# Optimization experiments

Hardware: AMD Instinct MI355X
Metric: run time of the kernel (lower is better)

Reference implementation:

```python
import jax, jax.numpy as jnp
import numpy as np

# Model dims (match init_kwargs / input_specs)
L = 2      # layer_dim
B = 64     # batch
T = 512    # max seq len
D = 256    # input_dim (== hidden_dim, required by stacked wiring)
H = 256    # hidden_dim
O = 2      # output_dim


def setup_inputs() -> dict:
    key = jax.random.key(0)
    ks = jax.random.split(key, 10)
    s = 1.0 / np.sqrt(H)
    f32 = jnp.float32
    return {
        "x_data": jax.random.normal(ks[0], (B, T, D), f32),
        "x_length": jax.random.randint(ks[1], (B,), 1, T + 1),
        "x_label": jax.random.uniform(ks[2], (B,), f32),
        # Per-layer GRU-cell weights, stacked over layers (bias=False).
        "Wz": (jax.random.normal(ks[3], (L, D, H), f32) * s),
        "Uz": (jax.random.normal(ks[4], (L, H, H), f32) * s),
        "Wr": (jax.random.normal(ks[5], (L, D, H), f32) * s),
        "Ur": (jax.random.normal(ks[6], (L, H, H), f32) * s),
        "Wh": (jax.random.normal(ks[7], (L, D, H), f32) * s),
        "Uh": (jax.random.normal(ks[8], (L, H, H), f32) * s),
        # Output projection of the last layer (only last layer's `out` is used).
        "Wo": (jax.random.normal(ks[9], (H, O), f32) * s),
    }


def reference(x_data, x_length, x_label, Wz, Uz, Wr, Ur, Wh, Uh, Wo):
    # Training-mode forward: sum over batch and valid timesteps of
    # (label - sigmoid(out[:, 1]))**2, with per-layer states S1, S2
    # carried across time. Vectorized over batch; lax.scan over time.
    Tn = x_data.shape[1]
    xs = jnp.swapaxes(x_data, 0, 1)  # [T, B, D]
    S1_0 = jnp.zeros((L, B, H), x_data.dtype)
    S2_0 = jnp.zeros((L, B, H), x_data.dtype)

    def step(carry, xt):
        S1, S2 = carry
        inp = xt  # [B, D]
        for l in range(L):  # small fixed layer loop
            z = jax.nn.sigmoid(inp @ Wz[l] + S1[l] @ Uz[l])
            r = jax.nn.sigmoid(inp @ Wr[l] + S1[l] @ Ur[l])
            h = jnp.tanh(inp @ Wh[l] + (r * S1[l]) @ Uh[l])
            hn = (1.0 - z) * S1[l] + z * h          # new hidden (S1)
            S2n = z * S2[l] + (1.0 - z) * h          # secondary memory (S2)
            S1 = S1.at[l].set(hn)
            S2 = S2.at[l].set(S2n)
            inp = hn
        score = jax.nn.sigmoid((inp @ Wo)[:, 1])     # out[:, 1] -> [B]
        return (S1, S2), score

    _, scores = jax.lax.scan(step, (S1_0, S2_0), xs)  # [T, B]
    mask = (jnp.arange(Tn)[:, None] < x_length[None, :]).astype(scores.dtype)
    loss = jnp.sum(mask * (x_label[None, :] - scores) ** 2)
    return loss
```

## Files before the change

kernel.cpp:

```cpp
#include <hip/hip_runtime.h>

#define LAY 2
#define BATCH 64
#define TMAX 512
#define DIM 256
#define AST 264
#define CHUNK 16

typedef float floatx4 __attribute__((ext_vector_type(4)));
typedef __bf16 bf16x8 __attribute__((ext_vector_type(8)));
#define MFMA_FP8  __builtin_amdgcn_mfma_f32_16x16x32_fp8_fp8
#define MFMA_BF16 __builtin_amdgcn_mfma_f32_16x16x32_bf16

#define BAR_LDS() asm volatile("s_waitcnt lgkmcnt(0)\n\ts_barrier" ::: "memory")

#define OFF_WPW 0xA0000
#define OFF_FLG 0x150000
#define OFF_XP  0x200000
#define OFF_HP  0x1C00000
#define OFF_HN  0x3600000

__device__ __forceinline__ unsigned short f2bf(float f) {
    unsigned int u = __float_as_uint(f);
    unsigned int r = u + 0x7fffu + ((u >> 16) & 1u);
    return (unsigned short)(r >> 16);
}
__device__ __forceinline__ unsigned int pk2(float a, float b) {
    return (unsigned int)__builtin_amdgcn_cvt_pk_fp8_f32(a, b, 0, false);
}
__device__ __forceinline__ unsigned char f2q(float a) { return (unsigned char)(pk2(a, a) & 0xff); }
__device__ __forceinline__ void unp4(unsigned int u, float* f) {
    auto lo = __builtin_amdgcn_cvt_pk_f32_fp8((int)u, false);
    auto hi = __builtin_amdgcn_cvt_pk_f32_fp8((int)u, true);
    f[0] = lo[0]; f[1] = lo[1]; f[2] = hi[0]; f[3] = hi[1];
}
__device__ __forceinline__ float sigf(float x) {
    return __builtin_amdgcn_rcpf(1.f + __expf(-x));
}
__device__ __forceinline__ float tanhfast2y(float twoy) { return 2.f * sigf(twoy) - 1.f; }

__device__ __forceinline__ void ast_u32(unsigned int* p, unsigned int v) {
    __hip_atomic_store(p, v, __ATOMIC_RELAXED, __HIP_MEMORY_SCOPE_AGENT);
}

__global__ void prep_weights(const float* __restrict__ Wz, const float* __restrict__ Wr,
                             const float* __restrict__ Wh, const float* __restrict__ Uz,
                             const float* __restrict__ Ur, const float* __restrict__ Uh,
                             unsigned char* __restrict__ ws, float* __restrict__ out) {
    int T = blockIdx.x * 256 + threadIdx.x;
    if (T == 0) out[0] = 0.f;
    if (T < 192) ((int*)(ws + OFF_FLG))[T] = 0;
    if (T < 294912) {
        int e = T & 3, half = (T >> 2) & 1, lane = (T >> 3) & 63;
        int kp = (T >> 9) & 3, nt = (T >> 11) & 15, mu = T >> 15;
        const float* s;
        if (mu < 6) {
            int g = mu % 3, l = mu / 3;
            s = (g == 0 ? Uz : g == 1 ? Ur : Uh) + l * 65536;
        } else {
            int g = mu - 6;
            s = (g == 0 ? Wz : g == 1 ? Wr : Wh) + 65536;
        }
        int n  = nt * 16 + (lane & 15);
        int k0 = (2 * kp + half) * 32 + (lane >> 4) * 8 + 2 * e;
        float w0 = s[(k0 << 8) + n] * 8.f;
        float w1 = s[((k0 + 1) << 8) + n] * 8.f;
        int addr = ((mu * 16 + nt) * 4 + kp) * 1024 + lane * 16 + half * 8 + 2 * e;
        *(unsigned short*)(ws + addr) = (unsigned short)(pk2(w0, w1) & 0xffff);
    } else {
        int T2 = T - 294912;
        int e = T2 & 3, lane = (T2 >> 2) & 63;
        int kf = (T2 >> 8) & 7, nt = (T2 >> 11) & 15, mw = T2 >> 15;
        const float* s = (mw == 0 ? Wz : mw == 1 ? Wr : Wh);
        int n  = nt * 16 + (lane & 15);
        int k0 = kf * 32 + (lane >> 4) * 8 + 2 * e;
        unsigned int v = (unsigned int)f2bf(s[(k0 << 8) + n]) |
                         ((unsigned int)f2bf(s[((k0 + 1) << 8) + n]) << 16);
        int addr = ((mw * 16 + nt) * 8 + kf) * 1024 + lane * 16 + 4 * e;
        *(unsigned int*)(ws + OFF_WPW + addr) = v;
    }
}

template <int SCORE, int WMODE, int POST>
__device__ __forceinline__ void scan_body(
    const unsigned int* __restrict__ xp, const unsigned char* __restrict__ wpU,
    int lbase, int bg, unsigned char* __restrict__ hnout,
    const int* __restrict__ xlen, const float* __restrict__ xlab,
    const float* __restrict__ Wo, float* __restrict__ out,
    int* wflags, int* pflag,
    unsigned char (*s1q)[AST], unsigned char (*rsq)[AST], float (*s1o)[264],
    float* wo1s, int* s_rdy, int tmax)
{
    const int tid = threadIdx.x, wave = tid >> 6, lane = tid & 63;
    const int l15 = lane & 15, quad = lane >> 4;
    const int b0 = bg * 16;

    for (int i = tid; i < 16 * AST; i += 1024) ((unsigned char*)s1q)[i] = 0;
    if (SCORE && tid < DIM) wo1s[tid] = Wo[2 * tid + 1];
    const int lenr = xlen[b0 + l15];
    const float labr = SCORE ? xlab[b0 + l15] : 0.f;
    (void)lenr; (void)labr;

    const int nt = wave;
    const int colA = nt * 16 + l15, rowb = quad * 4;

    long uz[8], ur[8], uh[8];
    {
        const unsigned char* pz = wpU + (size_t)(((lbase + 0) * 16 + nt) * 4) * 1024 + lane * 16;
        const unsigned char* pr = wpU + (size_t)(((lbase + 1) * 16 + nt) * 4) * 1024 + lane * 16;
        const unsigned char* ph = wpU + (size_t)(((lbase + 2) * 16 + nt) * 4) * 1024 + lane * 16;
#pragma unroll
        for (int kf = 0; kf < 8; ++kf) {
            int o = (kf >> 1) * 1024 + (kf & 1) * 8;
            uz[kf] = *(const long*)(pz + o);
            ur[kf] = *(const long*)(pr + o);
            uh[kf] = *(const long*)(ph + o);
        }
    }
    float s1r[4] = {};
    float accl = 0.f;
    int ready = 0;
    __syncthreads();

    for (int t = 0; t < tmax; ++t) {
        if constexpr (WMODE == 1) {
            if (t >= ready) {
                if (tid == 0) {
                    int vv, g = 0;
                    for (;;) {
                        vv = 1 << 30;
#pragma unroll
                        for (int q = 0; q < 4; ++q) {
                            int m = __hip_atomic_load(wflags + q, __ATOMIC_RELAXED, __HIP_MEMORY_SCOPE_AGENT);
                            vv = m < vv ? m : vv;
                        }
                        if (vv > t || ++g > (1 << 19)) break;
                        __builtin_amdgcn_s_sleep(2);
                    }
                    __threadfence();
                    *s_rdy = vv > t ? vv : t + 1;
                }
                __syncthreads();
                ready = *s_rdy;
            }
        } else if constexpr (WMODE == 2) {
            if (t >= ready) {
                if (tid == 0) {
                    const int ch = t >> 4;
                    int g = 0;
                    for (;;) {
                        int c = __hip_atomic_load(wflags + ch, __ATOMIC_RELAXED, __HIP_MEMORY_SCOPE_AGENT);
                        if (c >= 16 || ++g > (1 << 19)) break;
                        __builtin_amdgcn_s_sleep(2);
                    }
                    __threadfence();
                    *s_rdy = (ch + 1) * CHUNK;
                }
                __syncthreads();
                ready = *s_rdy;
            }
        }

        const unsigned int* xpt = xp + (size_t)(bg * 512 + t) * 3072 + lane;
        unsigned int xz = xpt[nt * 64];
        unsigned int xr = xpt[1024 + nt * 64];
        unsigned int xh = xpt[2048 + nt * 64];

        long sf[8];
#pragma unroll
        for (int kf = 0; kf < 8; ++kf) sf[kf] = *(const long*)&s1q[l15][kf * 32 + quad * 8];
        floatx4 za = {0.f, 0.f, 0.f, 0.f}, ra = za;
#pragma unroll
        for (int kf = 0; kf < 8; ++kf) {
            ra = MFMA_FP8(sf[kf], ur[kf], ra, 0, 0, 0);
            za = MFMA_FP8(sf[kf], uz[kf], za, 0, 0, 0);
        }
        float xrf[4];
        unp4(xr, xrf);
#pragma unroll
        for (int i = 0; i < 4; ++i) {
            float r = sigf(0.125f * ra[i] + 0.0625f * xrf[i]);
            rsq[rowb + i][colA] = f2q(r * s1r[i]);
        }
        BAR_LDS();

        long rf[8];
#pragma unroll
        for (int kf = 0; kf < 8; ++kf) rf[kf] = *(const long*)&rsq[l15][kf * 32 + quad * 8];
        floatx4 ha = {0.f, 0.f, 0.f, 0.f};
#pragma unroll
        for (int kf = 0; kf < 8; ++kf) ha = MFMA_FP8(rf[kf], uh[kf], ha, 0, 0, 0);
        float xzf[4], xhf[4];
        unp4(xz, xzf); unp4(xh, xhf);
#pragma unroll
        for (int i = 0; i < 4; ++i) {
            float z = sigf(0.125f * za[i] + 0.0625f * xzf[i]);
            float h = tanhfast2y(0.25f * ha[i] + 0.125f * xhf[i]);
            float hn = (1.f - z) * s1r[i] + z * h;
            s1r[i] = hn;
            s1q[rowb + i][colA] = f2q(hn);
            if (SCORE) s1o[rowb + i][colA] = hn;
        }
        BAR_LDS();

        if (!SCORE) {
            const int r = tid >> 6, c = (tid & 63) * 4;
            unsigned int v4 = *(const unsigned int*)&s1q[r][c];
            *(unsigned int*)(hnout + ((size_t)(b0 + r) * 512 + t) * 256 + c) = v4;
        } else if (wave == 0) {
            const int row = l15, c0 = quad * 64;
            float p = 0.f;
#pragma unroll
            for (int u = 0; u < 64; u += 4) {
                float4 sv = *(const float4*)&s1o[row][c0 + u];
                float4 wv = *(const float4*)&wo1s[c0 + u];
                p = fmaf(sv.x, wv.x, p); p = fmaf(sv.y, wv.y, p);
                p = fmaf(sv.z, wv.z, p); p = fmaf(sv.w, wv.w, p);
            }
            p += __shfl_xor(p, 16);
            p += __shfl_xor(p, 32);
            if (lane < 16 && t < lenr) {
                float sc = sigf(p);
                float d = labr - sc;
                accl = fmaf(d, d, accl);
            }
        }

        if (POST && (((t & (CHUNK - 1)) == (CHUNK - 1)) || t == tmax - 1)) {
            __syncthreads();
            if (tid == 0) {
                __threadfence();
                __hip_atomic_store(pflag, t + 1, __ATOMIC_RELEASE, __HIP_MEMORY_SCOPE_AGENT);
            }
        }
    }

    if (SCORE && wave == 0) {
        accl += __shfl_xor(accl, 1);
        accl += __shfl_xor(accl, 2);
        accl += __shfl_xor(accl, 4);
        accl += __shfl_xor(accl, 8);
        if (lane == 0) atomicAdd(out, accl);
    }
}

__global__ __launch_bounds__(1024, 4) void fused_pipeline(
    const float* __restrict__ x,
    unsigned int* __restrict__ XP, unsigned int* __restrict__ HP,
    const unsigned char* __restrict__ wpU, const unsigned char* __restrict__ wpW,
    unsigned char* __restrict__ HN,
    const int* __restrict__ xlen, const float* __restrict__ xlab,
    const float* __restrict__ Wo, float* __restrict__ out, int* flags)
{
    __shared__ __align__(16) unsigned char s1q[16][AST];
    __shared__ __align__(16) unsigned char rsq[16][AST];
    __shared__ __align__(16) float s1o[16][264];
    __shared__ float wo1s[DIM];
    __shared__ int s_rdy;

    const int bid = blockIdx.x;
    const int tid = threadIdx.x, wave = tid >> 6, lane = tid & 63;
    const int l15 = lane & 15, quad = lane >> 4;
    int* cnt = flags + 32;

    if (bid >= 24) {
        const int idx = bid - 24;
        const int pt = idx & 511, pbg = idx >> 9;
        const float* s = x + ((size_t)(pbg * 16 + l15) * 512 + pt) * 256;
        bf16x8 af[8];
#pragma unroll
        for (int kf = 0; kf < 8; ++kf) {
            float4 a = *(const float4*)(s + kf * 32 + quad * 8);
            float4 b = *(const float4*)(s + kf * 32 + quad * 8 + 4);
            union { unsigned short u[8]; bf16x8 v; } cv;
            cv.u[0] = f2bf(a.x); cv.u[1] = f2bf(a.y); cv.u[2] = f2bf(a.z); cv.u[3] = f2bf(a.w);
            cv.u[4] = f2bf(b.x); cv.u[5] = f2bf(b.y); cv.u[6] = f2bf(b.z); cv.u[7] = f2bf(b.w);
            af[kf] = cv.v;
        }
        floatx4 az = {0.f, 0.f, 0.f, 0.f}, ar = az, ah = az;
        const unsigned char* bz = wpW + (size_t)((0 * 16 + wave) * 8) * 1024 + lane * 16;
        const unsigned char* br = wpW + (size_t)((1 * 16 + wave) * 8) * 1024 + lane * 16;
        const unsigned char* bh = wpW + (size_t)((2 * 16 + wave) * 8) * 1024 + lane * 16;
#pragma unroll
        for (int kf = 0; kf < 8; ++kf) {
            az = MFMA_BF16(af[kf], *(const bf16x8*)(bz + kf * 1024), az, 0, 0, 0);
            ar = MFMA_BF16(af[kf], *(const bf16x8*)(br + kf * 1024), ar, 0, 0, 0);
            ah = MFMA_BF16(af[kf], *(const bf16x8*)(bh + kf * 1024), ah, 0, 0, 0);
        }
        const size_t ob = (size_t)(pbg * 512 + pt) * 3072 + wave * 64 + lane;
        ast_u32(&XP[ob],        pk2(16.f * az[0], 16.f * az[1]) | (pk2(16.f * az[2], 16.f * az[3]) << 16));
        ast_u32(&XP[ob + 1024], pk2(16.f * ar[0], 16.f * ar[1]) | (pk2(16.f * ar[2], 16.f * ar[3]) << 16));
        ast_u32(&XP[ob + 2048], pk2(16.f * ah[0], 16.f * ah[1]) | (pk2(16.f * ah[2], 16.f * ah[3]) << 16));
        __syncthreads();
        if (tid == 0)
            __hip_atomic_fetch_add(cnt + pbg * 32 + (pt >> 4), 1,
                                   __ATOMIC_RELAXED, __HIP_MEMORY_SCOPE_AGENT);
        return;
    }

    int role, bg, p = 0;
    if (bid < 4)       { role = 0; bg = bid; }
    else if (bid < 20) { role = 1; bg = (bid - 4) >> 2; p = (bid - 4) & 3; }
    else               { role = 2; bg = bid - 20; }
    const int b0 = bg * 16;

    int v = xlen[b0 + l15];
#pragma unroll
    for (int o = 1; o < 16; o <<= 1) v = max(v, __shfl_xor(v, o));
    const int tmax = __builtin_amdgcn_readfirstlane(v);

    if (role == 0) {
        scan_body<0, 2, 1>(XP, wpU, 0, bg, HN, xlen, xlab, Wo, out,
                           cnt + bg * 32, flags + bg, s1q, rsq, s1o, wo1s, &s_rdy, tmax);
    } else if (role == 2) {
        scan_body<1, 1, 0>(HP, wpU, 3, bg, nullptr, xlen, xlab, Wo, out,
                           flags + 4 + bg * 4, nullptr, s1q, rsq, s1o, wo1s, &s_rdy, tmax);
    } else {
        int* wf = flags + bg;
        int* pf = flags + 4 + bg * 4 + p;
        const unsigned char* bz = wpU + (size_t)((6 * 16 + wave) * 4) * 1024 + lane * 16;
        const unsigned char* br = wpU + (size_t)((7 * 16 + wave) * 4) * 1024 + lane * 16;
        const unsigned char* bh = wpU + (size_t)((8 * 16 + wave) * 4) * 1024 + lane * 16;
        for (int base = 0; base < tmax; base += CHUNK) {
            const int target = (base + CHUNK < tmax) ? base + CHUNK : tmax;
            if (tid == 0) {
                int vv, g = 0;
                for (;;) {
                    vv = __hip_atomic_load(wf, __ATOMIC_RELAXED, __HIP_MEMORY_SCOPE_AGENT);
                    if (vv >= target || ++g > (1 << 19)) break;
                    __builtin_amdgcn_s_sleep(2);
                }
                __threadfence();
            }
            __syncthreads();

            const int t0 = base + p * 4;
            const int t1 = (t0 + 4 < tmax) ? t0 + 4 : tmax;
            for (int t = t0; t < t1; ++t) {
                const unsigned char* sA = HN + ((size_t)(b0 + l15) * 512 + t) * 256;
                long af[8];
#pragma unroll
                for (int kf = 0; kf < 8; ++kf) af[kf] = *(const long*)(sA + kf * 32 + quad * 8);
                floatx4 az = {0.f, 0.f, 0.f, 0.f}, ar = az, ah = az;
#pragma unroll
                for (int kf = 0; kf < 8; ++kf) {
                    int o = (kf >> 1) * 1024 + (kf & 1) * 8;
                    az = MFMA_FP8(af[kf], *(const long*)(bz + o), az, 0, 0, 0);
                    ar = MFMA_FP8(af[kf], *(const long*)(br + o), ar, 0, 0, 0);
                    ah = MFMA_FP8(af[kf], *(const long*)(bh + o), ah, 0, 0, 0);
                }
                const size_t ob = (size_t)(bg * 512 + t) * 3072 + wave * 64 + lane;
                HP[ob]        = pk2(2.f * az[0], 2.f * az[1]) | (pk2(2.f * az[2], 2.f * az[3]) << 16);
                HP[ob + 1024] = pk2(2.f * ar[0], 2.f * ar[1]) | (pk2(2.f * ar[2], 2.f * ar[3]) << 16);
                HP[ob + 2048] = pk2(2.f * ah[0], 2.f * ah[1]) | (pk2(2.f * ah[2], 2.f * ah[3]) << 16);
            }

            __syncthreads();
            if (tid == 0) {
                __threadfence();
                __hip_atomic_store(pf, base + CHUNK, __ATOMIC_RELEASE, __HIP_MEMORY_SCOPE_AGENT);
            }
        }
    }
}

extern "C" void kernel_launch(void* const* d_in, const int* in_sizes, int n_in,
                              void* d_out, int out_size, void* d_ws, size_t ws_size,
                              hipStream_t stream) {
    const float* x    = (const float*)d_in[0];
    const int*   xlen = (const int*)d_in[1];
    const float* xlab = (const float*)d_in[2];
    const float* Wz   = (const float*)d_in[3];
    const float* Uz   = (const float*)d_in[4];
    const float* Wr   = (const float*)d_in[5];
    const float* Ur   = (const float*)d_in[6];
    const float* Wh   = (const float*)d_in[7];
    const float* Uh   = (const float*)d_in[8];
    const float* Wo   = (const float*)d_in[9];
    float* out = (float*)d_out;

    unsigned char* ws  = (unsigned char*)d_ws;
    unsigned char* wpU = ws;
    unsigned char* wpW = ws + OFF_WPW;
    int*           FLG = (int*)(ws + OFF_FLG);
    unsigned int*  XP  = (unsigned int*)(ws + OFF_XP);
    unsigned int*  HP  = (unsigned int*)(ws + OFF_HP);
    unsigned char* HN  = ws + OFF_HN;

    prep_weights<<<1536, 256, 0, stream>>>(Wz, Wr, Wh, Uz, Ur, Uh, ws, out);
    fused_pipeline<<<2072, 1024, 0, stream>>>(x, XP, HP, wpU, wpW, HN,
                                              xlen, xlab, Wo, out, FLG);
}
```

Measured before the change: 1.233 ms.

## Quantize recurrent weights in-kernel and interleave projected-input layout

The prep kernel no longer packs the FP8 U matrices or the layer-1 W matrices. Each scan and projection block now loads fp32 weights straight into registers and quantizes them once at startup, which shrinks the prep launch and drops a workspace round trip. The per-timestep XP/HP buffers are interleaved so the z, r and h values for a lane sit next to each other, and the hidden update uses an fma form. The trade-off is strided uncoalesced fp32 weight loads in every block's prologue, repeated across the many blocks.

Measured after the change: 1.126 ms. 8.7% less time.

```diff
diff --git a/kernel.cpp b/kernel.cpp
--- a/kernel.cpp
+++ b/kernel.cpp
@@ -43,48 +43,41 @@
     __hip_atomic_store(p, v, __ATOMIC_RELAXED, __HIP_MEMORY_SCOPE_AGENT);
 }
 
+__device__ __forceinline__ long quant8(const float* s) {
+    unsigned int p01 = pk2(8.f * s[0 * 256], 8.f * s[1 * 256]);
+    unsigned int p23 = pk2(8.f * s[2 * 256], 8.f * s[3 * 256]);
+    unsigned int p45 = pk2(8.f * s[4 * 256], 8.f * s[5 * 256]);
+    unsigned int p67 = pk2(8.f * s[6 * 256], 8.f * s[7 * 256]);
+    unsigned long long v = (unsigned long long)(p01 & 0xffffu)
+                         | ((unsigned long long)(p23 & 0xffffu) << 16)
+                         | ((unsigned long long)(p45 & 0xffffu) << 32)
+                         | ((unsigned long long)(p67 & 0xffffu) << 48);
+    return (long)v;
+}
+
 __global__ void prep_weights(const float* __restrict__ Wz, const float* __restrict__ Wr,
-                             const float* __restrict__ Wh, const float* __restrict__ Uz,
-                             const float* __restrict__ Ur, const float* __restrict__ Uh,
+                             const float* __restrict__ Wh,
                              unsigned char* __restrict__ ws, float* __restrict__ out) {
     int T = blockIdx.x * 256 + threadIdx.x;
     if (T == 0) out[0] = 0.f;
     if (T < 192) ((int*)(ws + OFF_FLG))[T] = 0;
-    if (T < 294912) {
-        int e = T & 3, half = (T >> 2) & 1, lane = (T >> 3) & 63;
-        int kp = (T >> 9) & 3, nt = (T >> 11) & 15, mu = T >> 15;
-        const float* s;
-        if (mu < 6) {
-            int g = mu % 3, l = mu / 3;
-            s = (g == 0 ? Uz : g == 1 ? Ur : Uh) + l * 65536;
-        } else {
-            int g = mu - 6;
-            s = (g == 0 ? Wz : g == 1 ? Wr : Wh) + 65536;
-        }
-        int n  = nt * 16 + (lane & 15);
-        int k0 = (2 * kp + half) * 32 + (lane >> 4) * 8 + 2 * e;
-        float w0 = s[(k0 << 8) + n] * 8.f;
-        float w1 = s[((k0 + 1) << 8) + n] * 8.f;
-        int addr = ((mu * 16 + nt) * 4 + kp) * 1024 + lane * 16 + half * 8 + 2 * e;
-        *(unsigned short*)(ws + addr) = (unsigned short)(pk2(w0, w1) & 0xffff);
-    } else {
-        int T2 = T - 294912;
-        int e = T2 & 3, lane = (T2 >> 2) & 63;
-        int kf = (T2 >> 8) & 7, nt = (T2 >> 11) & 15, mw = T2 >> 15;
-        const float* s = (mw == 0 ? Wz : mw == 1 ? Wr : Wh);
-        int n  = nt * 16 + (lane & 15);
-        int k0 = kf * 32 + (lane >> 4) * 8 + 2 * e;
-        unsigned int v = (unsigned int)f2bf(s[(k0 << 8) + n]) |
-                         ((unsigned int)f2bf(s[((k0 + 1) << 8) + n]) << 16);
-        int addr = ((mw * 16 + nt) * 8 + kf) * 1024 + lane * 16 + 4 * e;
-        *(unsigned int*)(ws + OFF_WPW + addr) = v;
-    }
+    int e = T & 3, lane = (T >> 2) & 63;
+    int kf = (T >> 8) & 7, nt = (T >> 11) & 15, mw = T >> 15;
+    const float* s = (mw == 0 ? Wz : mw == 1 ? Wr : Wh);
+    int n  = nt * 16 + (lane & 15);
+    int k0 = kf * 32 + (lane >> 4) * 8 + 2 * e;
+    unsigned int v = (unsigned int)f2bf(s[(k0 << 8) + n]) |
+                     ((unsigned int)f2bf(s[((k0 + 1) << 8) + n]) << 16);
+    int addr = ((mw * 16 + nt) * 8 + kf) * 1024 + lane * 16 + 4 * e;
+    *(unsigned int*)(ws + OFF_WPW + addr) = v;
 }
 
 template <int SCORE, int WMODE, int POST>
 __device__ __forceinline__ void scan_body(
-    const unsigned int* __restrict__ xp, const unsigned char* __restrict__ wpU,
-    int lbase, int bg, unsigned char* __restrict__ hnout,
+    const unsigned int* __restrict__ xp,
+    const float* __restrict__ Uzs, const float* __restrict__ Urs,
+    const float* __restrict__ Uhs,
+    int bg, unsigned char* __restrict__ hnout,
     const int* __restrict__ xlen, const float* __restrict__ xlab,
     const float* __restrict__ Wo, float* __restrict__ out,
     int* wflags, int* pflag,
@@ -106,15 +99,13 @@
 
     long uz[8], ur[8], uh[8];
     {
-        const unsigned char* pz = wpU + (size_t)(((lbase + 0) * 16 + nt) * 4) * 1024 + lane * 16;
-        const unsigned char* pr = wpU + (size_t)(((lbase + 1) * 16 + nt) * 4) * 1024 + lane * 16;
-        const unsigned char* ph = wpU + (size_t)(((lbase + 2) * 16 + nt) * 4) * 1024 + lane * 16;
+        const int nb = nt * 16 + l15;
 #pragma unroll
         for (int kf = 0; kf < 8; ++kf) {
-            int o = (kf >> 1) * 1024 + (kf & 1) * 8;
-            uz[kf] = *(const long*)(pz + o);
-            ur[kf] = *(const long*)(pr + o);
-            uh[kf] = *(const long*)(ph + o);
+            const size_t kb = (size_t)(kf * 32 + quad * 8) * 256 + nb;
+            uz[kf] = quant8(Uzs + kb);
+            ur[kf] = quant8(Urs + kb);
+            uh[kf] = quant8(Uhs + kb);
         }
     }
     float s1r[4] = {};
@@ -161,10 +152,10 @@
             }
         }
 
-        const unsigned int* xpt = xp + (size_t)(bg * 512 + t) * 3072 + lane;
-        unsigned int xz = xpt[nt * 64];
-        unsigned int xr = xpt[1024 + nt * 64];
-        unsigned int xh = xpt[2048 + nt * 64];
+        const unsigned int* xpt = xp + ((size_t)(bg * 512 + t) * 1024 + nt * 64 + lane) * 3;
+        unsigned int xz = xpt[0];
+        unsigned int xr = xpt[1];
+        unsigned int xh = xpt[2];
 
         long sf[8];
 #pragma unroll
@@ -196,7 +187,7 @@
         for (int i = 0; i < 4; ++i) {
             float z = sigf(0.125f * za[i] + 0.0625f * xzf[i]);
             float h = tanhfast2y(0.25f * ha[i] + 0.125f * xhf[i]);
-            float hn = (1.f - z) * s1r[i] + z * h;
+            float hn = fmaf(z, h - s1r[i], s1r[i]);
             s1r[i] = hn;
             s1q[rowb + i][colA] = f2q(hn);
             if (SCORE) s1o[rowb + i][colA] = hn;
@@ -247,10 +238,13 @@
 __global__ __launch_bounds__(1024, 4) void fused_pipeline(
     const float* __restrict__ x,
     unsigned int* __restrict__ XP, unsigned int* __restrict__ HP,
-    const unsigned char* __restrict__ wpU, const unsigned char* __restrict__ wpW,
-    unsigned char* __restrict__ HN,
+    const unsigned char* __restrict__ wpW, unsigned char* __restrict__ HN,
     const int* __restrict__ xlen, const float* __restrict__ xlab,
-    const float* __restrict__ Wo, float* __restrict__ out, int* flags)
+    const float* __restrict__ Wo, float* __restrict__ out, int* flags,
+    const float* __restrict__ Uz, const float* __restrict__ Ur,
+    const float* __restrict__ Uh,
+    const float* __restrict__ Wz, const float* __restrict__ Wr,
+    const float* __restrict__ Wh)
 {
     __shared__ __align__(16) unsigned char s1q[16][AST];
     __shared__ __align__(16) unsigned char rsq[16][AST];
@@ -287,10 +281,10 @@
             ar = MFMA_BF16(af[kf], *(const bf16x8*)(br + kf * 1024), ar, 0, 0, 0);
             ah = MFMA_BF16(af[kf], *(const bf16x8*)(bh + kf * 1024), ah, 0, 0, 0);
         }
-        const size_t ob = (size_t)(pbg * 512 + pt) * 3072 + wave * 64 + lane;
-        ast_u32(&XP[ob],        pk2(16.f * az[0], 16.f * az[1]) | (pk2(16.f * az[2], 16.f * az[3]) << 16));
-        ast_u32(&XP[ob + 1024], pk2(16.f * ar[0], 16.f * ar[1]) | (pk2(16.f * ar[2], 16.f * ar[3]) << 16));
-        ast_u32(&XP[ob + 2048], pk2(16.f * ah[0], 16.f * ah[1]) | (pk2(16.f * ah[2], 16.f * ah[3]) << 16));
+        const size_t ob3 = ((size_t)(pbg * 512 + pt) * 1024 + wave * 64 + lane) * 3;
+        ast_u32(&XP[ob3 + 0], pk2(16.f * az[0], 16.f * az[1]) | (pk2(16.f * az[2], 16.f * az[3]) << 16));
+        ast_u32(&XP[ob3 + 1], pk2(16.f * ar[0], 16.f * ar[1]) | (pk2(16.f * ar[2], 16.f * ar[3]) << 16));
+        ast_u32(&XP[ob3 + 2], pk2(16.f * ah[0], 16.f * ah[1]) | (pk2(16.f * ah[2], 16.f * ah[3]) << 16));
         __syncthreads();
         if (tid == 0)
             __hip_atomic_fetch_add(cnt + pbg * 32 + (pt >> 4), 1,
@@ -310,17 +304,27 @@
     const int tmax = __builtin_amdgcn_readfirstlane(v);
 
     if (role == 0) {
-        scan_body<0, 2, 1>(XP, wpU, 0, bg, HN, xlen, xlab, Wo, out,
+        scan_body<0, 2, 1>(XP, Uz, Ur, Uh, bg, HN, xlen, xlab, Wo, out,
                            cnt + bg * 32, flags + bg, s1q, rsq, s1o, wo1s, &s_rdy, tmax);
     } else if (role == 2) {
-        scan_body<1, 1, 0>(HP, wpU, 3, bg, nullptr, xlen, xlab, Wo, out,
+        scan_body<1, 1, 0>(HP, Uz + 65536, Ur + 65536, Uh + 65536, bg, nullptr,
+                           xlen, xlab, Wo, out,
                            flags + 4 + bg * 4, nullptr, s1q, rsq, s1o, wo1s, &s_rdy, tmax);
     } else {
         int* wf = flags + bg;
         int* pf = flags + 4 + bg * 4 + p;
-        const unsigned char* bz = wpU + (size_t)((6 * 16 + wave) * 4) * 1024 + lane * 16;
-        const unsigned char* br = wpU + (size_t)((7 * 16 + wave) * 4) * 1024 + lane * 16;
-        const unsigned char* bh = wpU + (size_t)((8 * 16 + wave) * 4) * 1024 + lane * 16;
+        const int nt = wave;
+        long wz1[8], wr1[8], wh1[8];
+        {
+            const int nb = nt * 16 + l15;
+#pragma unroll
+            for (int kf = 0; kf < 8; ++kf) {
+                const size_t kb = (size_t)(kf * 32 + quad * 8) * 256 + nb;
+                wz1[kf] = quant8(Wz + 65536 + kb);
+                wr1[kf] = quant8(Wr + 65536 + kb);
+                wh1[kf] = quant8(Wh + 65536 + kb);
+            }
+        }
         for (int base = 0; base < tmax; base += CHUNK) {
             const int target = (base + CHUNK < tmax) ? base + CHUNK : tmax;
             if (tid == 0) {
@@ -344,15 +348,14 @@
                 floatx4 az = {0.f, 0.f, 0.f, 0.f}, ar = az, ah = az;
 #pragma unroll
                 for (int kf = 0; kf < 8; ++kf) {
-                    int o = (kf >> 1) * 1024 + (kf & 1) * 8;
-                    az = MFMA_FP8(af[kf], *(const long*)(bz + o), az, 0, 0, 0);
-                    ar = MFMA_FP8(af[kf], *(const long*)(br + o), ar, 0, 0, 0);
-                    ah = MFMA_FP8(af[kf], *(const long*)(bh + o), ah, 0, 0, 0);
+                    az = MFMA_FP8(af[kf], wz1[kf], az, 0, 0, 0);
+                    ar = MFMA_FP8(af[kf], wr1[kf], ar, 0, 0, 0);
+                    ah = MFMA_FP8(af[kf], wh1[kf], ah, 0, 0, 0);
                 }
-                const size_t ob = (size_t)(bg * 512 + t) * 3072 + wave * 64 + lane;
-                HP[ob]        = pk2(2.f * az[0], 2.f * az[1]) | (pk2(2.f * az[2], 2.f * az[3]) << 16);
-                HP[ob + 1024] = pk2(2.f * ar[0], 2.f * ar[1]) | (pk2(2.f * ar[2], 2.f * ar[3]) << 16);
-                HP[ob + 2048] = pk2(2.f * ah[0], 2.f * ah[1]) | (pk2(2.f * ah[2], 2.f * ah[3]) << 16);
+                const size_t ob3 = ((size_t)(bg * 512 + t) * 1024 + nt * 64 + lane) * 3;
+                HP[ob3 + 0] = pk2(2.f * az[0], 2.f * az[1]) | (pk2(2.f * az[2], 2.f * az[3]) << 16);
+                HP[ob3 + 1] = pk2(2.f * ar[0], 2.f * ar[1]) | (pk2(2.f * ar[2], 2.f * ar[3]) << 16);
+                HP[ob3 + 2] = pk2(2.f * ah[0], 2.f * ah[1]) | (pk2(2.f * ah[2], 2.f * ah[3]) << 16);
             }
 
             __syncthreads();
@@ -380,14 +383,14 @@
     float* out = (float*)d_out;
 
     unsigned char* ws  = (unsigned char*)d_ws;
-    unsigned char* wpU = ws;
     unsigned char* wpW = ws + OFF_WPW;
     int*           FLG = (int*)(ws + OFF_FLG);
     unsigned int*  XP  = (unsigned int*)(ws + OFF_XP);
     unsigned int*  HP  = (unsigned int*)(ws + OFF_HP);
     unsigned char* HN  = ws + OFF_HN;
 
-    prep_weights<<<1536, 256, 0, stream>>>(Wz, Wr, Wh, Uz, Ur, Uh, ws, out);
-    fused_pipeline<<<2072, 1024, 0, stream>>>(x, XP, HP, wpU, wpW, HN,
-                                              xlen, xlab, Wo, out, FLG);
-}
+    prep_weights<<<384, 256, 0, stream>>>(Wz, Wr, Wh, ws, out);
+    fused_pipeline<<<2072, 1024, 0, stream>>>(x, XP, HP, wpW, HN,
+                                              xlen, xlab, Wo, out, FLG,
+                                              Uz, Ur, Uh, Wz, Wr, Wh);
+}
```
